# Kernel optimization log

Hardware: AMD Instinct MI355X
Metric: run time of the kernel (lower is better)

The kernel has to match this reference:

```python
import jax, jax.numpy as jnp
import numpy as np

KS = 7
ITERS = 6
B, C, H, W = 2, 64, 256, 1216

_WM7 = [1,1,1,1,1,1,1,1,0,0,0,0,0,1,1,0,0,0,0,0,1,1,0,0,0,0,0,1,1,0,0,0,0,0,1,1,0,0,0,0,0,1,1,1,1,1,1,1,1]
_WM5 = [0,0,0,0,0,0,0,0,1,1,1,1,1,0,0,1,0,0,0,1,0,0,1,0,0,0,1,0,0,1,0,0,0,1,0,0,1,1,1,1,1,0,0,0,0,0,0,0,0]
_WM3 = [0,0,0,0,0,0,0,0,0,0,0,0,0,0,0,0,1,1,1,0,0,0,0,1,0,1,0,0,0,0,1,1,1,0,0,0,0,0,0,0,0,0,0,0,0,0,0,0,0]

# per 7x7 position t: which guide tensor (ring) and which channel within it
_SRC = []
_i7 = _i5 = _i3 = 0
for _t in range(KS * KS):
    if _WM7[_t]:
        _SRC.append(("7", _i7)); _i7 += 1
    elif _WM5[_t]:
        _SRC.append(("5", _i5)); _i5 += 1
    elif _WM3[_t]:
        _SRC.append(("3", _i3)); _i3 += 1
    else:
        _SRC.append(("1", 0))


def _convbn(x, w, s, b):
    # Conv2d(bias=False) + BatchNorm2d (inference) folded to per-channel scale/bias.
    y = jax.lax.conv_general_dilated(x, w, window_strides=(1, 1),
                                     padding=((1, 1), (1, 1)),
                                     dimension_numbers=("NCHW", "OIHW", "NCHW"))
    return y * s[None, :, None, None] + b[None, :, None, None]


def setup_inputs() -> dict:
    key = jax.random.key(0)
    ks = iter(jax.random.split(key, 64))
    def nrm(shape, scale=1.0):
        return jax.random.normal(next(ks), shape, jnp.float32) * scale
    def uni(shape):
        return jax.random.uniform(next(ks), shape, dtype=jnp.float32)
    inp = {
        "feature": nrm((B, C, H, W)),
        "d0": uni((B, 1, H, W)),
        "d00": nrm((B, 1, H, W)),  # ~half positive -> mixed valid_mask
    }
    layers = [("aff7", 24), ("aff5", 16), ("aff3", 8),
              ("att7", 6), ("att5", 6), ("att3", 6), ("att1", 6), ("mask", 6)]
    fan = 1.0 / np.sqrt(C * 9)
    for name, out in layers:
        inp["w_" + name] = nrm((out, C, 3, 3), fan)
        inp["s_" + name] = uni((out,))
        inp["b_" + name] = nrm((out,), 0.1)
    return inp


def reference(feature, d0, d00,
              w_aff7, s_aff7, b_aff7, w_aff5, s_aff5, b_aff5, w_aff3, s_aff3, b_aff3,
              w_att7, s_att7, b_att7, w_att5, s_att5, b_att5, w_att3, s_att3, b_att3,
              w_att1, s_att1, b_att1, w_mask, s_mask, b_mask):
    valid = (d00 > 0).astype(d00.dtype)
    mask_all = jax.nn.sigmoid(_convbn(feature, w_mask, s_mask, b_mask)) * valid
    aff7 = _convbn(feature, w_aff7, s_aff7, b_aff7)  # [B,24,H,W]
    aff5 = _convbn(feature, w_aff5, s_aff5, b_aff5)  # [B,16,H,W]
    aff3 = _convbn(feature, w_aff3, s_aff3, b_aff3)  # [B, 8,H,W]
    att7 = jax.nn.sigmoid(_convbn(feature, w_att7, s_att7, b_att7))
    att5 = jax.nn.sigmoid(_convbn(feature, w_att5, s_att5, b_att5))
    att3 = jax.nn.sigmoid(_convbn(feature, w_att3, s_att3, b_att3))
    att1 = jax.nn.sigmoid(_convbn(feature, w_att1, s_att1, b_att1))

    dt = d0
    for it in range(ITERS):
        mask = mask_all[:, it:it + 1]
        g7 = att7[:, it:it + 1] * aff7
        g5 = att5[:, it:it + 1] * aff5
        g3 = att3[:, it:it + 1] * aff3
        g1 = att1[:, it:it + 1]
        denom = (jnp.sum(jnp.abs(g7), 1, keepdims=True)
                 + jnp.sum(jnp.abs(g5), 1, keepdims=True)
                 + jnp.sum(jnp.abs(g3), 1, keepdims=True)
                 + jnp.abs(g1))
        g7, g5, g3, g1 = g7 / denom, g5 / denom, g3 / denom, g1 / denom
        g0 = 1.0 - (jnp.sum(g7, 1, keepdims=True) + jnp.sum(g5, 1, keepdims=True)
                    + jnp.sum(g3, 1, keepdims=True) + g1)
        guides = {"7": g7, "5": g5, "3": g3, "1": g1}
        # scatter ring guides into full 49-channel 7x7 layout
        G = jnp.concatenate([guides[k][:, i:i + 1] for k, i in _SRC], axis=1)  # [B,49,H,W]
        # weighted neighbor gather: out(p) = sum_t G_t(p+off_t) * dt(p+off_t)
        P = G * dt  # [B,49,H,W]
        Pp = jnp.pad(P, ((0, 0), (0, 0), (3, 3), (3, 3)))
        acc = jnp.zeros_like(dt)
        for t in range(KS * KS):
            i, j = t // KS, t % KS
            acc = acc + Pp[:, t:t + 1, 6 - i:6 - i + H, 6 - j:6 - j + W]
        dt = acc + g0 * d0
        dt = mask * d00 + (1.0 - mask) * dt
    return dt
```

## Files before the change

kernel.cpp:

```cpp
#include <hip/hip_runtime.h>
#include <hip/hip_fp16.h>
#include <stdint.h>

#define HH 256
#define WW 1216
#define BB 2
#define CC 64
#define IPIX (HH*WW)
#define NPIX (BB*IPIX)

typedef __attribute__((ext_vector_type(8))) __bf16 bf16x8;
typedef __attribute__((ext_vector_type(4))) __bf16 bf16x4;
typedef __attribute__((ext_vector_type(4))) float floatx4;
typedef __attribute__((ext_vector_type(4))) _Float16 half4;
typedef __attribute__((ext_vector_type(4))) uint32_t uint32x4;

__device__ __forceinline__ float sigm(float x) { return 1.f / (1.f + __expf(-x)); }

constexpr int LSTART_H[9] = {0,24,40,48,54,60,66,72,78};

constexpr int PLANE[49] = {
  0, 1, 2, 3, 4, 5, 6,
  7,24,25,26,27,28, 8,
  9,29,40,41,42,30,10,
 11,31,43,-1,44,32,12,
 13,33,45,46,47,34,14,
 15,35,36,37,38,39,16,
 17,18,19,20,21,22,23};
constexpr int KCLS[49] = {
 0,0,0,0,0,0,0,
 0,1,1,1,1,1,0,
 0,1,2,2,2,1,0,
 0,1,2,3,2,1,0,
 0,1,2,2,2,1,0,
 0,1,1,1,1,1,0,
 0,0,0,0,0,0,0};
constexpr int TAPNC[48] = {
  0,1,2,3,4,5,6,7,8,9,10,11,12,13,14,15,16,17,18,19,20,21,22,23,
  25,26,27,28,29,30,31,32,33,34,35,36,37,38,39,40,41,42,43,44,45,46,47,48};

struct WPtrs {
    const float* w[8];
    const float* s[8];
    const float* b[8];
};

__global__ void k_pack(WPtrs wp, __bf16* __restrict__ wpk,
                       float* __restrict__ s_all, float* __restrict__ b_all) {
    int idx = blockIdx.x * blockDim.x + threadIdx.x;
    if (idx < 18 * 5 * 64) {
        int kk = idx / (5 * 64);
        int r = idx - kk * 5 * 64;
        int t = r >> 6, lane = r & 63;
        int m = t * 16 + (lane & 15);
        int L = 0, o = 0;
        bool valid_m = (m < 78);
        if (valid_m) {
            for (int i = 0; i < 8; i++) if (m >= LSTART_H[i]) { L = i; o = m - LSTART_H[i]; }
        }
        __bf16 vals[8];
        for (int j = 0; j < 8; j++) {
            int k = kk * 32 + ((lane >> 4) * 8) + j;
            int tap = k >> 6, c = k & 63;
            float w = valid_m ? wp.w[L][(o * 64 + c) * 9 + tap] : 0.f;
            vals[j] = (__bf16)w;
        }
        for (int j = 0; j < 8; j++) wpk[(size_t)idx * 8 + j] = vals[j];
    }
    if (idx < 80) {
        int m = idx;
        float sv = 0.f, bv = 0.f;
        if (m < 78) {
            int L = 0, o = 0;
            for (int i = 0; i < 8; i++) if (m >= LSTART_H[i]) { L = i; o = m - LSTART_H[i]; }
            sv = wp.s[L][o]; bv = wp.b[L][o];
        }
        s_all[m] = sv; b_all[m] = bv;
    }
}

__global__ __launch_bounds__(256) void k_cvt(const float* __restrict__ feat,
                                             __bf16* __restrict__ fpk) {
    const int x = blockIdx.x * 64 + (threadIdx.x & 63);
    const int half = threadIdx.x >> 6;
    const int y = blockIdx.y, b = blockIdx.z;
    const float* fb = feat + (size_t)b * CC * IPIX + (size_t)y * WW + x;
    __bf16* op = fpk + ((size_t)(b * IPIX + y * WW + x) << 6);
#pragma unroll
    for (int h = 0; h < 2; h++) {
        const int cg = half + h * 4;
        bf16x8 pk;
#pragma unroll
        for (int j = 0; j < 8; j++) pk[j] = (__bf16)fb[(size_t)(cg * 8 + j) * IPIX];
        *(bf16x8*)(op + cg * 8) = pk;
    }
}

__global__ __launch_bounds__(256, 4) void k_conv(const __bf16* __restrict__ fpk,
        const float* __restrict__ d00, const __bf16* __restrict__ wpk,
        const float* __restrict__ s_all, const float* __restrict__ b_all,
        __bf16* __restrict__ afx, __bf16* __restrict__ attp, __bf16* __restrict__ maskp,
        float* __restrict__ stp) {
    __shared__ __bf16 sh[6 * 34 * 72];
    __shared__ __bf16 wlds[2 * 2560];
    const int tid = threadIdx.x;
    int flat = blockIdx.x + 38 * (blockIdx.y + 64 * blockIdx.z);
    int nf = (flat & 7) * 608 + (flat >> 3);
    int bx = nf % 38; int r2 = nf / 38;
    const int x0 = bx * 32, y0 = (r2 & 63) * 4, b = r2 >> 6;

    {
        bf16x8 w0 = *(const bf16x8*)(wpk + (size_t)tid * 8);
        *(bf16x8*)(wlds + tid * 8) = w0;
        if (tid < 64) {
            bf16x8 w1 = *(const bf16x8*)(wpk + 2048 + (size_t)tid * 8);
            *(bf16x8*)(wlds + 2048 + tid * 8) = w1;
        }
    }
    for (int idx = tid; idx < 204 * 8; idx += 256) {
        int cg = idx & 7, pos = idx >> 3;
        int row = pos / 34, x = pos - row * 34;
        int gy = y0 + row - 1, gx = x0 + x - 1;
        bf16x8 pk;
#pragma unroll
        for (int j = 0; j < 8; j++) pk[j] = (__bf16)0.f;
        if (gy >= 0 && gy < HH && gx >= 0 && gx < WW)
            pk = *(const bf16x8*)(fpk + ((size_t)(b * IPIX + gy * WW + gx) << 6) + cg * 8);
        *(bf16x8*)(sh + pos * 72 + cg * 8) = pk;
    }
    __syncthreads();

    const int wave = tid >> 6, lane = tid & 63;
    const int n = lane & 15, g = lane >> 4;

    floatx4 acc[5][2];
#pragma unroll
    for (int t = 0; t < 5; t++)
#pragma unroll
        for (int q = 0; q < 2; q++) acc[t][q] = (floatx4)(0.f);

#pragma unroll
    for (int kk = 0; kk < 18; kk++) {
        bf16x8 wt0, wt1;
        if (kk < 17) {
            wt0 = *(const bf16x8*)(wpk + (size_t)(kk + 1) * 2560 + tid * 8);
            if (tid < 64) wt1 = *(const bf16x8*)(wpk + (size_t)(kk + 1) * 2560 + 2048 + tid * 8);
        }
        const int tap = kk >> 1;
        const int dy = tap / 3 - 1, dx = tap % 3 - 1;
        const int c0 = (kk & 1) * 32 + g * 8;
        bf16x8 bfr[2];
        const int rowb = wave + 1 + dy;
        const int colb = 1 + dx + n;
#pragma unroll
        for (int q = 0; q < 2; q++)
            bfr[q] = *(const bf16x8*)(sh + ((rowb * 34) + colb + q * 16) * 72 + c0);
        bf16x8 afr[5];
        const __bf16* wb = wlds + (kk & 1) * 2560 + lane * 8;
#pragma unroll
        for (int t = 0; t < 5; t++) afr[t] = *(const bf16x8*)(wb + t * 512);
#pragma unroll
        for (int t = 0; t < 5; t++)
#pragma unroll
            for (int q = 0; q < 2; q++)
                acc[t][q] = __builtin_amdgcn_mfma_f32_16x16x32_bf16(afr[t], bfr[q], acc[t][q], 0, 0, 0);
        if (kk < 17) {
            *(bf16x8*)(wlds + ((kk + 1) & 1) * 2560 + tid * 8) = wt0;
            if (tid < 64) *(bf16x8*)(wlds + ((kk + 1) & 1) * 2560 + 2048 + tid * 8) = wt1;
        }
        __syncthreads();
    }

    const int pix_base = b * IPIX + (y0 + wave) * WW + x0 + n;
    float p7[2] = {0,0}, t7[2] = {0,0};
    float p5[2] = {0,0}, t5[2] = {0,0};
    float p3[2] = {0,0}, t3[2] = {0,0};

#pragma unroll
    for (int t = 0; t < 5; t++) {
        const floatx4 sv = *(const floatx4*)(s_all + t * 16 + 4 * g);
        const floatx4 bv = *(const floatx4*)(b_all + t * 16 + 4 * g);
#pragma unroll
        for (int q = 0; q < 2; q++) {
#pragma unroll
            for (int reg = 0; reg < 4; reg++) {
                const int m = t * 16 + 4 * g + reg;
                const float v = fmaf(acc[t][q][reg], sv[reg], bv[reg]);
                if (m < 24)                { p7[q] += fabsf(v); t7[q] += v; }
                else if (m < 40)           { p5[q] += fabsf(v); t5[q] += v; }
                else if (m < 48)           { p3[q] += fabsf(v); t3[q] += v; }
                const float outv = (m < 48) ? v : sigm(v);
                sh[m * 132 + wave * 32 + n + q * 16] = (__bf16)outv;
            }
        }
    }
#pragma unroll
    for (int q = 0; q < 2; q++) {
        p7[q] += __shfl_xor(p7[q], 16); p7[q] += __shfl_xor(p7[q], 32);
        t7[q] += __shfl_xor(t7[q], 16); t7[q] += __shfl_xor(t7[q], 32);
        p5[q] += __shfl_xor(p5[q], 16); p5[q] += __shfl_xor(p5[q], 32);
        t5[q] += __shfl_xor(t5[q], 16); t5[q] += __shfl_xor(t5[q], 32);
        p3[q] += __shfl_xor(p3[q], 16); p3[q] += __shfl_xor(p3[q], 32);
        t3[q] += __shfl_xor(t3[q], 16); t3[q] += __shfl_xor(t3[q], 32);
    }
    if (g == 0) {
#pragma unroll
        for (int q = 0; q < 2; q++) {
            const int pixq = pix_base + q * 16;
            floatx4 s0 = {p7[q], p5[q], p3[q], t7[q]};
            floatx4 s1 = {t5[q], t3[q], 0.f, 0.f};
            *(floatx4*)(stp + (size_t)pixq * 8)     = s0;
            *(floatx4*)(stp + (size_t)pixq * 8 + 4) = s1;
        }
    }
    __syncthreads();

    {
        const int pxi = tid >> 1;
        const int hf = tid & 1;
        const int prow2 = pxi >> 5, pcol2 = pxi & 31;
        const int pix2 = b * IPIX + (y0 + prow2) * WW + x0 + pcol2;
#pragma unroll
        for (int k = 0; k < 3; k++) {
            bf16x8 v;
#pragma unroll
            for (int e = 0; e < 8; e++) {
                const int jj = hf * 24 + k * 8 + e;
                v[e] = sh[PLANE[TAPNC[jj]] * 132 + pxi];
            }
            *(bf16x8*)(afx + (size_t)pix2 * 48 + hf * 24 + k * 8) = v;
        }
    }

    const int px = tid & 127;
    const int grp = tid >> 7;
    const int prow = px >> 5, pcol = px & 31;
    const int pix = b * IPIX + (y0 + prow) * WW + x0 + pcol;
    const float d00v = d00[pix];
    const float valid = (d00v > 0.f) ? 1.f : 0.f;
#pragma unroll
    for (int j = 0; j < 6; j += 2) {
        const int it = j + grp;
        bf16x4 av = { sh[(48 + it) * 132 + px], sh[(54 + it) * 132 + px],
                      sh[(60 + it) * 132 + px], sh[(66 + it) * 132 + px] };
        *(bf16x4*)(attp + ((size_t)it * NPIX + pix) * 4) = av;
        maskp[(size_t)it * NPIX + pix] = (__bf16)((float)sh[(72 + it) * 132 + px] * valid);
    }
}

__global__ __launch_bounds__(256) void k_rg(const __bf16* __restrict__ attp,
        const float* __restrict__ stp, const float* __restrict__ d0,
        _Float16* __restrict__ rp, float* __restrict__ gd) {
    int g = blockIdx.x * blockDim.x + threadIdx.x;
    if (g >= NPIX) return;
    const floatx4 s0 = *(const floatx4*)(stp + (size_t)g * 8);
    const floatx4 s1 = *(const floatx4*)(stp + (size_t)g * 8 + 4);
    const float S7 = s0[0], S5 = s0[1], S3 = s0[2], T7 = s0[3], T5 = s1[0], T3 = s1[1];
    const float d0v = d0[g];
#pragma unroll
    for (int it = 0; it < 6; it++) {
        bf16x4 a = *(const bf16x4*)(attp + ((size_t)it * NPIX + g) * 4);
        float a7 = (float)a[0], a5 = (float)a[1], a3 = (float)a[2], a1 = (float)a[3];
        float denom = a7 * S7 + a5 * S5 + a3 * S3 + a1;
        float inv = 1.f / denom;
        float r7 = a7 * inv, r5 = a5 * inv, r3 = a3 * inv, r1 = a1 * inv;
        float g0 = 1.f - (r7 * T7 + r5 * T5 + r3 * T3 + r1);
        half4 rv = {(_Float16)r7, (_Float16)r5, (_Float16)r3, (_Float16)r1};
        *(half4*)(rp + ((size_t)it * NPIX + g) * 4) = rv;
        gd[(size_t)it * NPIX + g] = g0 * d0v;
    }
}

#define SPP 536
__global__ __launch_bounds__(256) void k_iter(const _Float16* __restrict__ rp,
        const float* __restrict__ gd, const float* __restrict__ dt,
        const __bf16* __restrict__ afx, const __bf16* __restrict__ maskp,
        const float* __restrict__ d00,
        float* __restrict__ dtn, int it) {
    __shared__ uint32_t sa32[532 * 25];
    __shared__ float sps[4 * SPP];
    const int tid = threadIdx.x;
    int flat = blockIdx.x + 38 * (blockIdx.y + 32 * blockIdx.z);
    int nf = (flat & 7) * 304 + (flat >> 3);
    int bx = nf % 38; int r2 = nf / 38;
    const int x0 = bx * 32, y0 = (r2 & 31) * 8, b = r2 >> 5;
    const int ib = b * IPIX;

    for (int idx = tid; idx < 532; idx += 256) {
        const int ly = idx / 38, lx = idx - ly * 38;
        const int gy = y0 + ly - 3, gx = x0 + lx - 3;
        uint32x4 A[6];
        float c0 = 0.f, c1 = 0.f, c2 = 0.f, c3 = 0.f;
        if (gy >= 0 && gy < HH && gx >= 0 && gx < WW) {
            const int q = ib + gy * WW + gx;
            const uint32_t* src = (const uint32_t*)(afx + (size_t)q * 48);
#pragma unroll
            for (int k = 0; k < 6; k++) A[k] = *(const uint32x4*)(src + k * 4);
            const half4 rv = *(const half4*)(rp + ((size_t)it * NPIX + q) * 4);
            const float dtv = dt[q];
            const float gdv = gd[(size_t)it * NPIX + q];
            c0 = (float)rv[0] * dtv; c1 = (float)rv[1] * dtv;
            c2 = (float)rv[2] * dtv; c3 = (float)rv[3] * dtv + gdv;
        } else {
#pragma unroll
            for (int k = 0; k < 6; k++) A[k] = (uint32x4)(0u);
        }
        uint32_t* d = sa32 + idx * 25;
#pragma unroll
        for (int k = 0; k < 6; k++) {
            d[k * 4 + 0] = A[k][0]; d[k * 4 + 1] = A[k][1];
            d[k * 4 + 2] = A[k][2]; d[k * 4 + 3] = A[k][3];
        }
        sps[idx] = c0; sps[SPP + idx] = c1; sps[2 * SPP + idx] = c2; sps[3 * SPP + idx] = c3;
    }
    __syncthreads();

    const int ox = tid & 31, oy = tid >> 5;
    const int pbase = oy * 38 + ox;
    const __bf16* sab = (const __bf16*)sa32;
    float acc0 = sps[3 * SPP + pbase + 3 * 38 + 3];
    float acc1 = 0.f;
#pragma unroll
    for (int jj = 0; jj < 48; jj++) {
        const int t = TAPNC[jj];
        const int i = t / 7, j = t % 7;
        const int off = (6 - i) * 38 + (6 - j);
        const float av = (float)sab[(pbase + off) * 50 + jj];
        const float pv = sps[KCLS[t] * SPP + pbase + off];
        if (jj & 1) acc1 = fmaf(av, pv, acc1);
        else        acc0 = fmaf(av, pv, acc0);
    }
    const float acc = acc0 + acc1;

    const int pix = ib + (y0 + oy) * WW + (x0 + ox);
    const float m = (float)maskp[(size_t)it * NPIX + pix];
    dtn[pix] = m * d00[pix] + (1.f - m) * acc;
}

extern "C" void kernel_launch(void* const* d_in, const int* in_sizes, int n_in,
                              void* d_out, int out_size, void* d_ws, size_t ws_size,
                              hipStream_t stream) {
    const float* feat = (const float*)d_in[0];
    const float* d0   = (const float*)d_in[1];
    const float* d00  = (const float*)d_in[2];
    WPtrs wp;
    for (int l = 0; l < 8; l++) {
        wp.w[l] = (const float*)d_in[3 + 3 * l];
        wp.s[l] = (const float*)d_in[4 + 3 * l];
        wp.b[l] = (const float*)d_in[5 + 3 * l];
    }
    __bf16*   wsb   = (__bf16*)d_ws;
    __bf16*   afx   = wsb;
    __bf16*   attp  = afx + (size_t)48 * NPIX;
    __bf16*   msk_b = attp + (size_t)24 * NPIX;
    float*    stp   = (float*)(msk_b + (size_t)6 * NPIX);
    float*    dtA   = stp + (size_t)8 * NPIX;
    __bf16*   wpk   = (__bf16*)(dtA + (size_t)NPIX);
    float*    s_all = (float*)(wpk + 18 * 5 * 64 * 8);
    float*    b_all = s_all + 80;
    char*     X     = (char*)(b_all + 80);
    __bf16*   fpk   = (__bf16*)X;
    _Float16* rp    = (_Float16*)X;
    float*    gd    = (float*)(X + (size_t)24 * NPIX * 2);
    float*    dtB   = (float*)d_out;

    hipLaunchKernelGGL(k_pack, dim3(23), dim3(256), 0, stream, wp, wpk, s_all, b_all);
    hipLaunchKernelGGL(k_cvt, dim3(WW / 64, HH, BB), dim3(256), 0, stream, feat, fpk);
    hipLaunchKernelGGL(k_conv, dim3(38, 64, 2), dim3(256), 0, stream,
                       fpk, d00, wpk, s_all, b_all, afx, attp, msk_b, stp);
    hipLaunchKernelGGL(k_rg, dim3(NPIX / 256), dim3(256), 0, stream,
                       attp, stp, d0, rp, gd);
    const float* cur = d0;
    for (int it = 0; it < 6; ++it) {
        float* nxt = (it & 1) ? dtB : dtA;
        if (it == 5) nxt = dtB;
        hipLaunchKernelGGL(k_iter, dim3(38, 32, 2), dim3(256), 0, stream,
                           rp, gd, cur, afx, msk_b, d00, nxt, it);
        cur = nxt;
    }
}
```

Measured before the change: 559.0 us.

## Fuse propagation iterations into persistent kernel with grid barrier and pre-transposed affinities

Replaces the six per-iteration launches with one persistent kernel of 1216 blocks. Each thread keeps its two pixels' 48 affinity taps in registers across all iterations, and an atomic grid barrier separates iterations. A new transpose kernel pre-gathers each pixel's neighbour-shifted affinity values so the iteration loop no longer reloads affinity halos. The separate bf16 conversion kernel is removed and the conv loads fp32 features directly. The grid barrier depends on all 1216 blocks being co-resident, and it has a spin-count timeout that could break correctness silently.

```diff
diff --git a/kernel.cpp b/kernel.cpp
--- a/kernel.cpp
+++ b/kernel.cpp
@@ -8,12 +8,12 @@
 #define CC 64
 #define IPIX (HH*WW)
 #define NPIX (BB*IPIX)
+#define NBLK 1216
 
 typedef __attribute__((ext_vector_type(8))) __bf16 bf16x8;
 typedef __attribute__((ext_vector_type(4))) __bf16 bf16x4;
 typedef __attribute__((ext_vector_type(4))) float floatx4;
 typedef __attribute__((ext_vector_type(4))) _Float16 half4;
-typedef __attribute__((ext_vector_type(4))) uint32_t uint32x4;
 
 __device__ __forceinline__ float sigm(float x) { return 1.f / (1.f + __expf(-x)); }
 
@@ -46,8 +46,10 @@
 };
 
 __global__ void k_pack(WPtrs wp, __bf16* __restrict__ wpk,
-                       float* __restrict__ s_all, float* __restrict__ b_all) {
+                       float* __restrict__ s_all, float* __restrict__ b_all,
+                       int* __restrict__ bar) {
     int idx = blockIdx.x * blockDim.x + threadIdx.x;
+    if (idx < 8) bar[idx] = 0;
     if (idx < 18 * 5 * 64) {
         int kk = idx / (5 * 64);
         int r = idx - kk * 5 * 64;
@@ -79,24 +81,7 @@
     }
 }
 
-__global__ __launch_bounds__(256) void k_cvt(const float* __restrict__ feat,
-                                             __bf16* __restrict__ fpk) {
-    const int x = blockIdx.x * 64 + (threadIdx.x & 63);
-    const int half = threadIdx.x >> 6;
-    const int y = blockIdx.y, b = blockIdx.z;
-    const float* fb = feat + (size_t)b * CC * IPIX + (size_t)y * WW + x;
-    __bf16* op = fpk + ((size_t)(b * IPIX + y * WW + x) << 6);
-#pragma unroll
-    for (int h = 0; h < 2; h++) {
-        const int cg = half + h * 4;
-        bf16x8 pk;
-#pragma unroll
-        for (int j = 0; j < 8; j++) pk[j] = (__bf16)fb[(size_t)(cg * 8 + j) * IPIX];
-        *(bf16x8*)(op + cg * 8) = pk;
-    }
-}
-
-__global__ __launch_bounds__(256, 4) void k_conv(const __bf16* __restrict__ fpk,
+__global__ __launch_bounds__(256, 4) void k_conv(const float* __restrict__ feat,
         const float* __restrict__ d00, const __bf16* __restrict__ wpk,
         const float* __restrict__ s_all, const float* __restrict__ b_all,
         __bf16* __restrict__ afx, __bf16* __restrict__ attp, __bf16* __restrict__ maskp,
@@ -117,16 +102,22 @@
             *(bf16x8*)(wlds + 2048 + tid * 8) = w1;
         }
     }
-    for (int idx = tid; idx < 204 * 8; idx += 256) {
-        int cg = idx & 7, pos = idx >> 3;
-        int row = pos / 34, x = pos - row * 34;
-        int gy = y0 + row - 1, gx = x0 + x - 1;
-        bf16x8 pk;
-#pragma unroll
-        for (int j = 0; j < 8; j++) pk[j] = (__bf16)0.f;
-        if (gy >= 0 && gy < HH && gx >= 0 && gx < WW)
-            pk = *(const bf16x8*)(fpk + ((size_t)(b * IPIX + gy * WW + gx) << 6) + cg * 8);
-        *(bf16x8*)(sh + pos * 72 + cg * 8) = pk;
+    {
+        const float* fb = feat + (size_t)b * CC * IPIX;
+        for (int idx = tid; idx < 204 * 8; idx += 256) {
+            int pos = idx % 204, cg = idx / 204;
+            int row = pos / 34, x = pos - row * 34;
+            int gy = y0 + row - 1, gx = x0 + x - 1;
+            bf16x8 pk;
+#pragma unroll
+            for (int j = 0; j < 8; j++) pk[j] = (__bf16)0.f;
+            if (gy >= 0 && gy < HH && gx >= 0 && gx < WW) {
+                const float* fp0 = fb + (size_t)(cg * 8) * IPIX + (size_t)gy * WW + gx;
+#pragma unroll
+                for (int j = 0; j < 8; j++) pk[j] = (__bf16)fp0[(size_t)j * IPIX];
+            }
+            *(bf16x8*)(sh + pos * 72 + cg * 8) = pk;
+        }
     }
     __syncthreads();
 
@@ -245,6 +236,47 @@
                       sh[(60 + it) * 132 + px], sh[(66 + it) * 132 + px] };
         *(bf16x4*)(attp + ((size_t)it * NPIX + pix) * 4) = av;
         maskp[(size_t)it * NPIX + pix] = (__bf16)((float)sh[(72 + it) * 132 + px] * valid);
+    }
+}
+
+__global__ __launch_bounds__(256) void k_trans(const __bf16* __restrict__ afx,
+                                               __bf16* __restrict__ afy) {
+    __shared__ unsigned short rec[532 * 50];
+    const int tid = threadIdx.x;
+    int flat = blockIdx.x + 38 * (blockIdx.y + 32 * blockIdx.z);
+    int nf = (flat & 7) * 304 + (flat >> 3);
+    int bx = nf % 38; int r2 = nf / 38;
+    const int x0 = bx * 32, y0 = (r2 & 31) * 8, b = r2 >> 5;
+    const int ib = b * IPIX;
+
+    const uint32_t* afx32 = (const uint32_t*)afx;
+    uint32_t* rec32 = (uint32_t*)rec;
+    for (int idx = tid; idx < 532 * 24; idx += 256) {
+        const int d = idx % 24, rc = idx / 24;
+        const int ly = rc / 38, lx = rc - ly * 38;
+        const int gy = y0 + ly - 3, gx = x0 + lx - 3;
+        uint32_t v = 0u;
+        if (gy >= 0 && gy < HH && gx >= 0 && gx < WW)
+            v = afx32[(size_t)(ib + gy * WW + gx) * 24 + d];
+        rec32[rc * 25 + d] = v;
+    }
+    __syncthreads();
+
+    const int pcol = tid & 31, prow = tid >> 5;
+    const int pix = ib + (y0 + prow) * WW + x0 + pcol;
+    const __bf16* recb = (const __bf16*)rec;
+#pragma unroll
+    for (int k = 0; k < 6; k++) {
+        bf16x8 v;
+#pragma unroll
+        for (int e = 0; e < 8; e++) {
+            const int jj = k * 8 + e;
+            const int t = TAPNC[jj];
+            const int i = t / 7, j = t % 7;
+            const int rc = (prow + 6 - i) * 38 + (pcol + 6 - j);
+            v[e] = recb[rc * 50 + jj];
+        }
+        *(bf16x8*)(afy + (size_t)pix * 48 + k * 8) = v;
     }
 }
 
@@ -271,70 +303,115 @@
     }
 }
 
-#define SPP 536
-__global__ __launch_bounds__(256) void k_iter(const _Float16* __restrict__ rp,
-        const float* __restrict__ gd, const float* __restrict__ dt,
-        const __bf16* __restrict__ afx, const __bf16* __restrict__ maskp,
+#define SPL 984
+__global__ __launch_bounds__(256, 5) void k_pers(const _Float16* __restrict__ rp,
+        const float* __restrict__ gd, const float* __restrict__ d0,
+        const __bf16* __restrict__ afy, const __bf16* __restrict__ maskp,
         const float* __restrict__ d00,
-        float* __restrict__ dtn, int it) {
-    __shared__ uint32_t sa32[532 * 25];
-    __shared__ float sps[4 * SPP];
+        float* __restrict__ dtA, float* __restrict__ dtB, int* __restrict__ bar) {
+    __shared__ float sps[4 * SPL];
     const int tid = threadIdx.x;
-    int flat = blockIdx.x + 38 * (blockIdx.y + 32 * blockIdx.z);
-    int nf = (flat & 7) * 304 + (flat >> 3);
-    int bx = nf % 38; int r2 = nf / 38;
-    const int x0 = bx * 32, y0 = (r2 & 31) * 8, b = r2 >> 5;
+    const int id = blockIdx.x;
+    const int nf = (id & 7) * 152 + (id >> 3);
+    const int b = nf / 608; const int r = nf - b * 608;
+    const int by = r / 19, bx = r - by * 19;
+    const int x0 = bx * 64, y0 = by * 8;
     const int ib = b * IPIX;
-
-    for (int idx = tid; idx < 532; idx += 256) {
-        const int ly = idx / 38, lx = idx - ly * 38;
-        const int gy = y0 + ly - 3, gx = x0 + lx - 3;
-        uint32x4 A[6];
-        float c0 = 0.f, c1 = 0.f, c2 = 0.f, c3 = 0.f;
-        if (gy >= 0 && gy < HH && gx >= 0 && gx < WW) {
-            const int q = ib + gy * WW + gx;
-            const uint32_t* src = (const uint32_t*)(afx + (size_t)q * 48);
-#pragma unroll
-            for (int k = 0; k < 6; k++) A[k] = *(const uint32x4*)(src + k * 4);
-            const half4 rv = *(const half4*)(rp + ((size_t)it * NPIX + q) * 4);
-            const float dtv = dt[q];
-            const float gdv = gd[(size_t)it * NPIX + q];
-            c0 = (float)rv[0] * dtv; c1 = (float)rv[1] * dtv;
-            c2 = (float)rv[2] * dtv; c3 = (float)rv[3] * dtv + gdv;
-        } else {
-#pragma unroll
-            for (int k = 0; k < 6; k++) A[k] = (uint32x4)(0u);
-        }
-        uint32_t* d = sa32 + idx * 25;
-#pragma unroll
-        for (int k = 0; k < 6; k++) {
-            d[k * 4 + 0] = A[k][0]; d[k * 4 + 1] = A[k][1];
-            d[k * 4 + 2] = A[k][2]; d[k * 4 + 3] = A[k][3];
-        }
-        sps[idx] = c0; sps[SPP + idx] = c1; sps[2 * SPP + idx] = c2; sps[3 * SPP + idx] = c3;
-    }
-    __syncthreads();
-
-    const int ox = tid & 31, oy = tid >> 5;
-    const int pbase = oy * 38 + ox;
-    const __bf16* sab = (const __bf16*)sa32;
-    float acc0 = sps[3 * SPP + pbase + 3 * 38 + 3];
-    float acc1 = 0.f;
-#pragma unroll
-    for (int jj = 0; jj < 48; jj++) {
-        const int t = TAPNC[jj];
-        const int i = t / 7, j = t % 7;
-        const int off = (6 - i) * 38 + (6 - j);
-        const float av = (float)sab[(pbase + off) * 50 + jj];
-        const float pv = sps[KCLS[t] * SPP + pbase + off];
-        if (jj & 1) acc1 = fmaf(av, pv, acc1);
-        else        acc0 = fmaf(av, pv, acc0);
-    }
-    const float acc = acc0 + acc1;
-
-    const int pix = ib + (y0 + oy) * WW + (x0 + ox);
-    const float m = (float)maskp[(size_t)it * NPIX + pix];
-    dtn[pix] = m * d00[pix] + (1.f - m) * acc;
+    const int ox = tid & 63, py = tid >> 6;
+
+    const int pixA = ib + (y0 + py) * WW + x0 + ox;
+    const int pixB = pixA + 4 * WW;
+
+    const __bf16* ra = afy + (size_t)pixA * 48;
+    const __bf16* rb = afy + (size_t)pixB * 48;
+    bf16x8 Aa0 = *(const bf16x8*)(ra),      Aa1 = *(const bf16x8*)(ra + 8);
+    bf16x8 Aa2 = *(const bf16x8*)(ra + 16), Aa3 = *(const bf16x8*)(ra + 24);
+    bf16x8 Aa4 = *(const bf16x8*)(ra + 32), Aa5 = *(const bf16x8*)(ra + 40);
+    bf16x8 Ab0 = *(const bf16x8*)(rb),      Ab1 = *(const bf16x8*)(rb + 8);
+    bf16x8 Ab2 = *(const bf16x8*)(rb + 16), Ab3 = *(const bf16x8*)(rb + 24);
+    bf16x8 Ab4 = *(const bf16x8*)(rb + 32), Ab5 = *(const bf16x8*)(rb + 40);
+    const float dva = d00[pixA], dvb = d00[pixB];
+
+    auto recdot = [&](bf16x8 A0, bf16x8 A1, bf16x8 A2, bf16x8 A3, bf16x8 A4, bf16x8 A5,
+                      int cb) -> float {
+        float a0 = sps[3 * SPL + cb + 3 * 70 + 3];
+        float a1 = 0.f, a2 = 0.f, a3 = 0.f;
+#pragma unroll
+        for (int jj = 0; jj < 48; jj++) {
+            const int t = TAPNC[jj];
+            const int i = t / 7, j = t % 7;
+            const int off = (6 - i) * 70 + (6 - j);
+            float av;
+            switch (jj >> 3) {
+                case 0: av = (float)A0[jj & 7]; break;
+                case 1: av = (float)A1[jj & 7]; break;
+                case 2: av = (float)A2[jj & 7]; break;
+                case 3: av = (float)A3[jj & 7]; break;
+                case 4: av = (float)A4[jj & 7]; break;
+                default: av = (float)A5[jj & 7]; break;
+            }
+            const float pv = sps[KCLS[t] * SPL + cb + off];
+            switch (jj & 3) {
+                case 0: a0 = fmaf(av, pv, a0); break;
+                case 1: a1 = fmaf(av, pv, a1); break;
+                case 2: a2 = fmaf(av, pv, a2); break;
+                default: a3 = fmaf(av, pv, a3); break;
+            }
+        }
+        return (a0 + a1) + (a2 + a3);
+    };
+
+#pragma unroll
+    for (int it = 0; it < 6; it++) {
+        const float* src = (it == 0) ? d0 : ((it & 1) ? dtA : dtB);
+        float* dst = (it & 1) ? dtB : dtA;
+
+#pragma unroll
+        for (int r4 = 0; r4 < 4; r4++) {
+            const int idx = tid + r4 * 256;
+            if (idx < 980) {
+                const int ly = idx / 70, lx = idx - ly * 70;
+                const int gy = y0 + ly - 3, gx = x0 + lx - 3;
+                float c0 = 0.f, c1 = 0.f, c2 = 0.f, c3 = 0.f;
+                if (gy >= 0 && gy < HH && gx >= 0 && gx < WW) {
+                    const int q = ib + gy * WW + gx;
+                    const half4 rv = *(const half4*)(rp + ((size_t)it * NPIX + q) * 4);
+                    const float dtv = src[q];
+                    const float gdv = gd[(size_t)it * NPIX + q];
+                    c0 = (float)rv[0] * dtv; c1 = (float)rv[1] * dtv;
+                    c2 = (float)rv[2] * dtv; c3 = (float)rv[3] * dtv + gdv;
+                }
+                sps[idx] = c0; sps[SPL + idx] = c1;
+                sps[2 * SPL + idx] = c2; sps[3 * SPL + idx] = c3;
+            }
+        }
+        __syncthreads();
+
+        const int cbA = py * 70 + ox;
+        const float accA = recdot(Aa0, Aa1, Aa2, Aa3, Aa4, Aa5, cbA);
+        const float accB = recdot(Ab0, Ab1, Ab2, Ab3, Ab4, Ab5, cbA + 4 * 70);
+        const float ma = (float)maskp[(size_t)it * NPIX + pixA];
+        const float mb = (float)maskp[(size_t)it * NPIX + pixB];
+        dst[pixA] = ma * dva + (1.f - ma) * accA;
+        dst[pixB] = mb * dvb + (1.f - mb) * accB;
+
+        if (it < 5) {
+            __syncthreads();
+            __threadfence();
+            if (tid == 0) {
+                __hip_atomic_fetch_add(&bar[it], 1, __ATOMIC_ACQ_REL,
+                                       __HIP_MEMORY_SCOPE_AGENT);
+                int spins = 0;
+                while (__hip_atomic_load(&bar[it], __ATOMIC_ACQUIRE,
+                                         __HIP_MEMORY_SCOPE_AGENT) < NBLK) {
+                    __builtin_amdgcn_s_sleep(8);
+                    if (++spins > (1 << 20)) break;
+                }
+            }
+            __syncthreads();
+            __threadfence();
+        }
+    }
 }
 
 extern "C" void kernel_launch(void* const* d_in, const int* in_sizes, int n_in,
@@ -350,32 +427,27 @@
         wp.b[l] = (const float*)d_in[5 + 3 * l];
     }
     __bf16*   wsb   = (__bf16*)d_ws;
-    __bf16*   afx   = wsb;
-    __bf16*   attp  = afx + (size_t)48 * NPIX;
+    __bf16*   afy   = wsb;
+    __bf16*   attp  = afy + (size_t)48 * NPIX;
     __bf16*   msk_b = attp + (size_t)24 * NPIX;
     float*    stp   = (float*)(msk_b + (size_t)6 * NPIX);
     float*    dtA   = stp + (size_t)8 * NPIX;
     __bf16*   wpk   = (__bf16*)(dtA + (size_t)NPIX);
     float*    s_all = (float*)(wpk + 18 * 5 * 64 * 8);
     float*    b_all = s_all + 80;
-    char*     X     = (char*)(b_all + 80);
-    __bf16*   fpk   = (__bf16*)X;
-    _Float16* rp    = (_Float16*)X;
-    float*    gd    = (float*)(X + (size_t)24 * NPIX * 2);
+    int*      bar   = (int*)(b_all + 80);
+    char*     Y     = (char*)(bar + 16);
+    __bf16*   afx   = (__bf16*)Y;
+    _Float16* rp    = (_Float16*)Y;
+    float*    gd    = (float*)(Y + (size_t)24 * NPIX * 2);
     float*    dtB   = (float*)d_out;
 
-    hipLaunchKernelGGL(k_pack, dim3(23), dim3(256), 0, stream, wp, wpk, s_all, b_all);
-    hipLaunchKernelGGL(k_cvt, dim3(WW / 64, HH, BB), dim3(256), 0, stream, feat, fpk);
+    hipLaunchKernelGGL(k_pack, dim3(23), dim3(256), 0, stream, wp, wpk, s_all, b_all, bar);
     hipLaunchKernelGGL(k_conv, dim3(38, 64, 2), dim3(256), 0, stream,
-                       fpk, d00, wpk, s_all, b_all, afx, attp, msk_b, stp);
+                       feat, d00, wpk, s_all, b_all, afx, attp, msk_b, stp);
+    hipLaunchKernelGGL(k_trans, dim3(38, 32, 2), dim3(256), 0, stream, afx, afy);
     hipLaunchKernelGGL(k_rg, dim3(NPIX / 256), dim3(256), 0, stream,
                        attp, stp, d0, rp, gd);
-    const float* cur = d0;
-    for (int it = 0; it < 6; ++it) {
-        float* nxt = (it & 1) ? dtB : dtA;
-        if (it == 5) nxt = dtB;
-        hipLaunchKernelGGL(k_iter, dim3(38, 32, 2), dim3(256), 0, stream,
-                           rp, gd, cur, afx, msk_b, d00, nxt, it);
-        cur = nxt;
-    }
-}
+    hipLaunchKernelGGL(k_pers, dim3(NBLK), dim3(256), 0, stream,
+                       rp, gd, d0, afy, msk_b, d00, dtA, (float*)d_out, bar);
+}
```

New measurement: 2.116 ms. +278.6%, slower.
